# Kernel optimization log

Hardware: AMD Instinct MI355X
Metric: run time of the kernel (lower is better)

## Reference

```python
import jax, jax.numpy as jnp
import numpy as np
from jax import lax

B, L, H, K = 256, 512, 768, 64


def setup_inputs() -> dict:
    key = jax.random.key(0)
    k1, k2, k3, k4, k5 = jax.random.split(key, 5)
    features = jax.random.normal(k1, (B, L, H), dtype=jnp.float32)
    W = jax.random.normal(k2, (H, K), dtype=jnp.float32) * 0.02
    b = jnp.zeros((K,), dtype=jnp.float32)
    transition = jax.random.normal(k3, (K, K), dtype=jnp.float32)
    tags = jax.random.randint(k4, (B, L), 0, K, dtype=jnp.int64)
    # variable sentence lengths in decreasing order (repo sorts batches by length)
    lengths = jnp.sort(jax.random.randint(k5, (B,), L // 4, L + 1))[::-1]
    mask = jnp.arange(L)[None, :] < lengths[:, None]  # (B, L) bool, pads at end
    return {"features": features, "W": W, "b": b, "transition": transition,
            "tags": tags, "mask": mask}


def reference(features, W, b, transition, tags, mask):
    # encode: hidden2tag linear (dropout is identity in eval)
    emit = jnp.einsum("blh,hk->blk", features, W) + b  # (B, L, K)
    maskf = mask.astype(emit.dtype)

    # gold path score
    gold_emit = jnp.take_along_axis(emit, tags[:, :, None], axis=2)[..., 0]  # (B, L)
    trans_sc = transition[tags[:, :-1], tags[:, 1:]]                          # (B, L-1)
    score = gold_emit.at[:, 1:].add(trans_sc)
    total_score = (score * maskf).sum(axis=1)                                 # (B,)

    # CRF forward algorithm (log partition) via scan over time
    d0 = emit[:, 0]  # (B, K)
    emit_t = jnp.moveaxis(emit[:, 1:], 1, 0)  # (L-1, B, K)
    mask_t = mask[:, 1:].T                    # (L-1, B)

    def step(d, xs):
        e_t, m_t = xs
        # log_sum[b, j, k] = d[b, j] + transition[j, k] + e_t[b, k]
        log_sum = d[:, :, None] + transition[None, :, :] + e_t[:, None, :]
        d_new = jax.scipy.special.logsumexp(log_sum, axis=1)  # (B, K)
        d = jnp.where(m_t[:, None], d_new, d)  # finished sequences keep old d
        return d, None

    d, _ = lax.scan(step, d0, (emit_t, mask_t))
    log_z = jax.scipy.special.logsumexp(d, axis=1)  # (B,)

    return log_z - total_score  # negative log-likelihood per sentence, (B,)
```

## Files before the change

### kernel.cpp

```cpp
#include <hip/hip_runtime.h>
#include <hip/hip_bf16.h>
#include <string.h>

#define B_ 256
#define L_ 512
#define H_ 768
#define K_ 64

typedef float  float4v  __attribute__((ext_vector_type(4)));
typedef short  short8v  __attribute__((ext_vector_type(8)));

union BFragU { uint4 u4; short8v s8; };

__device__ inline unsigned short f2bf_bits(float f) {
    union { float f; unsigned int u; } c; c.f = f;
    unsigned int u = c.u;
    u += 0x7fffu + ((u >> 16) & 1u);
    return (unsigned short)(u >> 16);
}

#define WT_STRIDE 408

__global__ __launch_bounds__(256, 2)
void emit_gemm(const float* __restrict__ A, const float* __restrict__ W,
               const float* __restrict__ bias, float* __restrict__ emit) {
    __shared__ __align__(16) unsigned short Wt[64 * WT_STRIDE];
    const int tid  = threadIdx.x;
    const int lane = tid & 63;
    const int wid  = tid >> 6;
    const int lm   = lane & 15;
    const int lq   = lane >> 4;

    float4v acc[4][4];
    #pragma unroll
    for (int c = 0; c < 4; ++c)
        #pragma unroll
        for (int nt = 0; nt < 4; ++nt)
            acc[c][nt] = (float4v)0.f;

    for (int half = 0; half < 2; ++half) {
        __syncthreads();
        for (int i = tid; i < 384 * 64; i += 256) {
            int h = i >> 6, k = i & 63;
            Wt[k * WT_STRIDE + h] = f2bf_bits(W[(half * 384 + h) * 64 + k]);
        }
        __syncthreads();

        #pragma unroll 2
        for (int ks = 0; ks < 12; ++ks) {
            short8v bfrag[4];
            #pragma unroll
            for (int nt = 0; nt < 4; ++nt) {
                const unsigned short* p =
                    &Wt[(lm + nt * 16) * WT_STRIDE + ks * 32 + lq * 8];
                BFragU bb; bb.u4 = *reinterpret_cast<const uint4*>(p);
                bfrag[nt] = bb.s8;
            }
            #pragma unroll
            for (int c = 0; c < 4; ++c) {
                int row = (blockIdx.x * 4 + c) * 64 + wid * 16 + lm;
                const float* ap = A + (size_t)row * H_ + half * 384 + ks * 32 + lq * 8;
                float4 a0 = *reinterpret_cast<const float4*>(ap);
                float4 a1 = *reinterpret_cast<const float4*>(ap + 4);
                __hip_bfloat162 tt[4];
                tt[0] = __float22bfloat162_rn(make_float2(a0.x, a0.y));
                tt[1] = __float22bfloat162_rn(make_float2(a0.z, a0.w));
                tt[2] = __float22bfloat162_rn(make_float2(a1.x, a1.y));
                tt[3] = __float22bfloat162_rn(make_float2(a1.z, a1.w));
                short8v afrag;
                memcpy(&afrag, tt, 16);
                #pragma unroll
                for (int nt = 0; nt < 4; ++nt)
                    acc[c][nt] = __builtin_amdgcn_mfma_f32_16x16x32_bf16(
                        afrag, bfrag[nt], acc[c][nt], 0, 0, 0);
            }
        }
    }

    float bv[4];
    #pragma unroll
    for (int nt = 0; nt < 4; ++nt) bv[nt] = bias[nt * 16 + lm];
    #pragma unroll
    for (int c = 0; c < 4; ++c) {
        int rowb = (blockIdx.x * 4 + c) * 64 + wid * 16 + lq * 4;
        #pragma unroll
        for (int nt = 0; nt < 4; ++nt) {
            int col = nt * 16 + lm;
            #pragma unroll
            for (int r = 0; r < 4; ++r)
                emit[(size_t)(rowb + r) * 64 + col] = acc[c][nt][r] + bv[nt];
        }
    }
}

__global__ __launch_bounds__(64, 1)
void crf_scan(const float* __restrict__ emit, const float* __restrict__ T,
              const int* __restrict__ tags, const int* __restrict__ mask,
              float* __restrict__ out) {
    const int b    = blockIdx.x;
    const int lane = threadIdx.x;
    __shared__ __align__(16) float pbuf[2][64];

    int len = 0;
    #pragma unroll
    for (int j = 0; j < 8; ++j) len += (mask[b * L_ + j * 64 + lane] != 0);
    #pragma unroll
    for (int off = 32; off > 0; off >>= 1) len += __shfl_xor(len, off, 64);

    float et[64];
    #pragma unroll
    for (int i = 0; i < 64; ++i) et[i] = __expf(T[i * 64 + lane]);

    const float* eb = emit + (size_t)b * L_ * 64;

    float sc = 0.f;
    for (int t = lane; t < len; t += 64) {
        int tg = tags[b * L_ + t];
        sc += eb[(size_t)t * 64 + tg];
        if (t > 0) sc += T[tags[b * L_ + t - 1] * 64 + tg];
    }
    #pragma unroll
    for (int off = 32; off > 0; off >>= 1) sc += __shfl_xor(sc, off, 64);

    float d = eb[lane];
    for (int t = 1; t < len; ++t) {
        float e = eb[(size_t)t * 64 + lane];
        float m = __int_as_float(__builtin_amdgcn_readfirstlane(__float_as_int(d)));
        float p = __expf(d - m);
        float* pb = pbuf[t & 1];
        pb[lane] = p;
        const float4* pb4 = reinterpret_cast<const float4*>(pb);
        float a0 = 0.f, a1 = 0.f, a2 = 0.f, a3 = 0.f;
        #pragma unroll
        for (int i = 0; i < 16; ++i) {
            float4 pv = pb4[i];
            a0 += pv.x * et[i * 4 + 0];
            a1 += pv.y * et[i * 4 + 1];
            a2 += pv.z * et[i * 4 + 2];
            a3 += pv.w * et[i * 4 + 3];
        }
        float s = (a0 + a1) + (a2 + a3);
        d = m + e + __logf(s);
    }

    float mx = d;
    #pragma unroll
    for (int off = 32; off > 0; off >>= 1) mx = fmaxf(mx, __shfl_xor(mx, off, 64));
    float z = __expf(d - mx);
    #pragma unroll
    for (int off = 32; off > 0; off >>= 1) z += __shfl_xor(z, off, 64);
    if (lane == 0) out[b] = mx + __logf(z) - sc;
}

extern "C" void kernel_launch(void* const* d_in, const int* in_sizes, int n_in,
                              void* d_out, int out_size, void* d_ws, size_t ws_size,
                              hipStream_t stream) {
    const float* feat = (const float*)d_in[0];
    const float* W    = (const float*)d_in[1];
    const float* bias = (const float*)d_in[2];
    const float* T    = (const float*)d_in[3];
    const int*   tags = (const int*)d_in[4];
    const int*   mask = (const int*)d_in[5];
    float* out  = (float*)d_out;
    float* emit = (float*)d_ws;

    hipLaunchKernelGGL(emit_gemm, dim3(512), dim3(256), 0, stream, feat, W, bias, emit);
    hipLaunchKernelGGL(crf_scan,  dim3(B_),  dim3(64),  0, stream, emit, T, tags, mask, out);
}
```

Measured before the change: 741.3 us.

## Pre-transpose W globally, shrink GEMM tiles, restructure CRF scan with scaled probabilities

A separate small kernel converts W to a transposed bf16 layout in workspace, so the GEMM no longer builds a shared-memory copy in every block. The GEMM now uses 128-row tiles across 1024 blocks with higher occupancy. The CRF scan drops the per-step exp/log and keeps scaled probabilities, tracking the scale through the exponent of the previous sum. It also prefetches emission rows in 16-step chunks into double-buffered shared memory and uses packed float2 FMAs. This shortens the serial per-step chain, at the cost of some numeric-stability risk from the exponent-only rescaling.

```diff
diff --git a/kernel.cpp b/kernel.cpp
--- a/kernel.cpp
+++ b/kernel.cpp
@@ -6,8 +6,10 @@
 #define L_ 512
 #define H_ 768
 #define K_ 64
+#define WT_OFF 33554432
 
 typedef float  float4v  __attribute__((ext_vector_type(4)));
+typedef float  float2v  __attribute__((ext_vector_type(2)));
 typedef short  short8v  __attribute__((ext_vector_type(8)));
 
 union BFragU { uint4 u4; short8v s8; };
@@ -19,61 +21,60 @@
     return (unsigned short)(u >> 16);
 }
 
-#define WT_STRIDE 408
-
-__global__ __launch_bounds__(256, 2)
-void emit_gemm(const float* __restrict__ A, const float* __restrict__ W,
+__device__ inline float2v mk2(float x, float y) { float2v v; v.x = x; v.y = y; return v; }
+
+__global__ void wt_transpose(const float* __restrict__ W, unsigned int* __restrict__ Wt) {
+    int k = blockIdx.x;
+    int j = threadIdx.x;
+    float a = W[(size_t)(2 * j) * K_ + k];
+    float b = W[(size_t)(2 * j + 1) * K_ + k];
+    unsigned int u = (unsigned int)f2bf_bits(a) | ((unsigned int)f2bf_bits(b) << 16);
+    Wt[k * (H_ / 2) + j] = u;
+}
+
+__global__ __launch_bounds__(256, 4)
+void emit_gemm(const float* __restrict__ A, const unsigned short* __restrict__ Wt,
                const float* __restrict__ bias, float* __restrict__ emit) {
-    __shared__ __align__(16) unsigned short Wt[64 * WT_STRIDE];
     const int tid  = threadIdx.x;
     const int lane = tid & 63;
     const int wid  = tid >> 6;
     const int lm   = lane & 15;
     const int lq   = lane >> 4;
 
-    float4v acc[4][4];
-    #pragma unroll
-    for (int c = 0; c < 4; ++c)
+    float4v acc[2][4];
+    #pragma unroll
+    for (int c = 0; c < 2; ++c)
         #pragma unroll
         for (int nt = 0; nt < 4; ++nt)
             acc[c][nt] = (float4v)0.f;
 
-    for (int half = 0; half < 2; ++half) {
-        __syncthreads();
-        for (int i = tid; i < 384 * 64; i += 256) {
-            int h = i >> 6, k = i & 63;
-            Wt[k * WT_STRIDE + h] = f2bf_bits(W[(half * 384 + h) * 64 + k]);
-        }
-        __syncthreads();
-
-        #pragma unroll 2
-        for (int ks = 0; ks < 12; ++ks) {
-            short8v bfrag[4];
+    const int rowbase = blockIdx.x * 128 + wid * 16 + lm;
+
+    for (int ks = 0; ks < 24; ++ks) {
+        short8v bfrag[4];
+        #pragma unroll
+        for (int nt = 0; nt < 4; ++nt) {
+            const uint4* bp = reinterpret_cast<const uint4*>(
+                Wt + (size_t)(lm + nt * 16) * H_ + ks * 32 + lq * 8);
+            BFragU bb; bb.u4 = *bp;
+            bfrag[nt] = bb.s8;
+        }
+        #pragma unroll
+        for (int c = 0; c < 2; ++c) {
+            const float* ap = A + (size_t)(rowbase + c * 64) * H_ + ks * 32 + lq * 8;
+            float4 a0 = *reinterpret_cast<const float4*>(ap);
+            float4 a1 = *reinterpret_cast<const float4*>(ap + 4);
+            __hip_bfloat162 tt[4];
+            tt[0] = __float22bfloat162_rn(make_float2(a0.x, a0.y));
+            tt[1] = __float22bfloat162_rn(make_float2(a0.z, a0.w));
+            tt[2] = __float22bfloat162_rn(make_float2(a1.x, a1.y));
+            tt[3] = __float22bfloat162_rn(make_float2(a1.z, a1.w));
+            short8v afrag;
+            memcpy(&afrag, tt, 16);
             #pragma unroll
-            for (int nt = 0; nt < 4; ++nt) {
-                const unsigned short* p =
-                    &Wt[(lm + nt * 16) * WT_STRIDE + ks * 32 + lq * 8];
-                BFragU bb; bb.u4 = *reinterpret_cast<const uint4*>(p);
-                bfrag[nt] = bb.s8;
-            }
-            #pragma unroll
-            for (int c = 0; c < 4; ++c) {
-                int row = (blockIdx.x * 4 + c) * 64 + wid * 16 + lm;
-                const float* ap = A + (size_t)row * H_ + half * 384 + ks * 32 + lq * 8;
-                float4 a0 = *reinterpret_cast<const float4*>(ap);
-                float4 a1 = *reinterpret_cast<const float4*>(ap + 4);
-                __hip_bfloat162 tt[4];
-                tt[0] = __float22bfloat162_rn(make_float2(a0.x, a0.y));
-                tt[1] = __float22bfloat162_rn(make_float2(a0.z, a0.w));
-                tt[2] = __float22bfloat162_rn(make_float2(a1.x, a1.y));
-                tt[3] = __float22bfloat162_rn(make_float2(a1.z, a1.w));
-                short8v afrag;
-                memcpy(&afrag, tt, 16);
-                #pragma unroll
-                for (int nt = 0; nt < 4; ++nt)
-                    acc[c][nt] = __builtin_amdgcn_mfma_f32_16x16x32_bf16(
-                        afrag, bfrag[nt], acc[c][nt], 0, 0, 0);
-            }
+            for (int nt = 0; nt < 4; ++nt)
+                acc[c][nt] = __builtin_amdgcn_mfma_f32_16x16x32_bf16(
+                    afrag, bfrag[nt], acc[c][nt], 0, 0, 0);
         }
     }
 
@@ -81,14 +82,14 @@
     #pragma unroll
     for (int nt = 0; nt < 4; ++nt) bv[nt] = bias[nt * 16 + lm];
     #pragma unroll
-    for (int c = 0; c < 4; ++c) {
-        int rowb = (blockIdx.x * 4 + c) * 64 + wid * 16 + lq * 4;
+    for (int c = 0; c < 2; ++c) {
+        int rowb = blockIdx.x * 128 + c * 64 + wid * 16 + lq * 4;
         #pragma unroll
         for (int nt = 0; nt < 4; ++nt) {
             int col = nt * 16 + lm;
             #pragma unroll
             for (int r = 0; r < 4; ++r)
-                emit[(size_t)(rowb + r) * 64 + col] = acc[c][nt][r] + bv[nt];
+                emit[(size_t)(rowb + r) * K_ + col] = acc[c][nt][r] + bv[nt];
         }
     }
 }
@@ -99,57 +100,94 @@
               float* __restrict__ out) {
     const int b    = blockIdx.x;
     const int lane = threadIdx.x;
-    __shared__ __align__(16) float pbuf[2][64];
+    __shared__ __align__(16) float ebuf[2][16 * 64];
+    __shared__ __align__(16) float qbuf[2][64];
 
     int len = 0;
     #pragma unroll
     for (int j = 0; j < 8; ++j) len += (mask[b * L_ + j * 64 + lane] != 0);
     #pragma unroll
-    for (int off = 32; off > 0; off >>= 1) len += __shfl_xor(len, off, 64);
-
-    float et[64];
-    #pragma unroll
-    for (int i = 0; i < 64; ++i) et[i] = __expf(T[i * 64 + lane]);
-
-    const float* eb = emit + (size_t)b * L_ * 64;
+    for (int off = 32; off; off >>= 1) len += __shfl_xor(len, off, 64);
+
+    float2v et2[32];
+    #pragma unroll
+    for (int j = 0; j < 32; ++j) {
+        et2[j].x = __expf(T[(2 * j) * K_ + lane]);
+        et2[j].y = __expf(T[(2 * j + 1) * K_ + lane]);
+    }
+
+    const float* eb = emit + (size_t)b * L_ * K_;
 
     float sc = 0.f;
     for (int t = lane; t < len; t += 64) {
         int tg = tags[b * L_ + t];
-        sc += eb[(size_t)t * 64 + tg];
-        if (t > 0) sc += T[tags[b * L_ + t - 1] * 64 + tg];
-    }
-    #pragma unroll
-    for (int off = 32; off > 0; off >>= 1) sc += __shfl_xor(sc, off, 64);
-
-    float d = eb[lane];
-    for (int t = 1; t < len; ++t) {
-        float e = eb[(size_t)t * 64 + lane];
-        float m = __int_as_float(__builtin_amdgcn_readfirstlane(__float_as_int(d)));
-        float p = __expf(d - m);
-        float* pb = pbuf[t & 1];
-        pb[lane] = p;
-        const float4* pb4 = reinterpret_cast<const float4*>(pb);
-        float a0 = 0.f, a1 = 0.f, a2 = 0.f, a3 = 0.f;
-        #pragma unroll
-        for (int i = 0; i < 16; ++i) {
-            float4 pv = pb4[i];
-            a0 += pv.x * et[i * 4 + 0];
-            a1 += pv.y * et[i * 4 + 1];
-            a2 += pv.z * et[i * 4 + 2];
-            a3 += pv.w * et[i * 4 + 3];
-        }
-        float s = (a0 + a1) + (a2 + a3);
-        d = m + e + __logf(s);
-    }
-
-    float mx = d;
-    #pragma unroll
-    for (int off = 32; off > 0; off >>= 1) mx = fmaxf(mx, __shfl_xor(mx, off, 64));
-    float z = __expf(d - mx);
-    #pragma unroll
-    for (int off = 32; off > 0; off >>= 1) z += __shfl_xor(z, off, 64);
-    if (lane == 0) out[b] = mx + __logf(z) - sc;
+        sc += eb[(size_t)t * K_ + tg];
+        if (t > 0) sc += T[tags[b * L_ + t - 1] * K_ + tg];
+    }
+    #pragma unroll
+    for (int off = 32; off; off >>= 1) sc += __shfl_xor(sc, off, 64);
+
+    float e00 = eb[lane];
+    float M = __int_as_float(__builtin_amdgcn_readfirstlane(__float_as_int(e00)));
+    float q = __expf(e00 - M);
+    qbuf[0][lane] = q;
+    int prev_eps = 0;
+
+    const int soff = ((lane >> 2) << 6) + ((lane & 3) << 4);
+    {
+        const float4* src = reinterpret_cast<const float4*>(eb + soff);
+        float4 r0 = src[0], r1 = src[1], r2 = src[2], r3 = src[3];
+        float4* dst = reinterpret_cast<float4*>(&ebuf[0][soff]);
+        dst[0] = r0; dst[1] = r1; dst[2] = r2; dst[3] = r3;
+    }
+
+    int cur = 0;
+    int t = 1;
+    for (int c = 0;; ++c) {
+        const int nt0  = (c + 1) << 4;
+        const bool more = nt0 < len;
+        float4 r0, r1, r2, r3;
+        if (more) {
+            const float4* src = reinterpret_cast<const float4*>(eb + nt0 * K_ + soff);
+            r0 = src[0]; r1 = src[1]; r2 = src[2]; r3 = src[3];
+        }
+        const int tend = more ? nt0 : len;
+        for (; t < tend; ++t) {
+            float e  = ebuf[cur][((t & 15) << 6) + lane];
+            float ef = __int_as_float(__builtin_amdgcn_readfirstlane(__float_as_int(e)));
+            float delta = (float)prev_eps * 0.69314718f + ef;
+            M += delta;
+            float f = __expf(e - delta);
+
+            const float4* qb4 = reinterpret_cast<const float4*>(&qbuf[(t + 1) & 1][0]);
+            float2v a0 = mk2(0.f, 0.f), a1 = mk2(0.f, 0.f);
+            float2v a2 = mk2(0.f, 0.f), a3 = mk2(0.f, 0.f);
+            #pragma unroll
+            for (int r = 0; r < 16; r += 2) {
+                float4 p0 = qb4[r];
+                float4 p1 = qb4[r + 1];
+                a0 += mk2(p0.x, p0.y) * et2[2 * r];
+                a1 += mk2(p0.z, p0.w) * et2[2 * r + 1];
+                a2 += mk2(p1.x, p1.y) * et2[2 * r + 2];
+                a3 += mk2(p1.z, p1.w) * et2[2 * r + 3];
+            }
+            float2v s2 = (a0 + a1) + (a2 + a3);
+            float s = s2.x + s2.y;
+            unsigned su = (unsigned)__builtin_amdgcn_readfirstlane(__float_as_int(s));
+            prev_eps = (int)((su >> 23) & 0xff) - 127;
+            q = s * f;
+            qbuf[t & 1][lane] = q;
+        }
+        if (!more) break;
+        float4* dst = reinterpret_cast<float4*>(&ebuf[cur ^ 1][soff]);
+        dst[0] = r0; dst[1] = r1; dst[2] = r2; dst[3] = r3;
+        cur ^= 1;
+    }
+
+    float z = q;
+    #pragma unroll
+    for (int off = 32; off; off >>= 1) z += __shfl_xor(z, off, 64);
+    if (lane == 0) out[b] = M + __logf(z) - sc;
 }
 
 extern "C" void kernel_launch(void* const* d_in, const int* in_sizes, int n_in,
@@ -163,7 +201,10 @@
     const int*   mask = (const int*)d_in[5];
     float* out  = (float*)d_out;
     float* emit = (float*)d_ws;
-
-    hipLaunchKernelGGL(emit_gemm, dim3(512), dim3(256), 0, stream, feat, W, bias, emit);
-    hipLaunchKernelGGL(crf_scan,  dim3(B_),  dim3(64),  0, stream, emit, T, tags, mask, out);
-}
+    unsigned int*   WtW = (unsigned int*)((char*)d_ws + WT_OFF);
+    unsigned short* Wt  = (unsigned short*)WtW;
+
+    hipLaunchKernelGGL(wt_transpose, dim3(K_),   dim3(H_ / 2), 0, stream, W, WtW);
+    hipLaunchKernelGGL(emit_gemm,    dim3(1024), dim3(256),    0, stream, feat, Wt, bias, emit);
+    hipLaunchKernelGGL(crf_scan,     dim3(B_),   dim3(64),     0, stream, emit, T, tags, mask, out);
+}
```

New measurement: 745.6 us. About the same (+0.6%).
